# Performance work log

Measured on AMD Instinct MI355X. Metric: run time of the kernel, lower is better.

The kernel has to match this reference:

```python
import jax, jax.numpy as jnp
import numpy as np

VOCAB = 100000
EMBED = 64
B, S, K = 1024, 50, 20


def setup_inputs() -> dict:
    key = jax.random.key(0)
    k1, k2, k3 = jax.random.split(key, 3)
    content_input = jax.random.randint(k1, (B, S, K), 0, VOCAB)
    # nn.Linear(vocab_size, embed_size): weight [E, V], bias [E]
    W = jax.random.normal(k2, (EMBED, VOCAB), dtype=jnp.float32) * 0.02
    b = jax.random.normal(k3, (EMBED,), dtype=jnp.float32) * 0.02
    return {"content_input": content_input, "W": W, "b": b}


def reference(content_input, W, b):
    # Original: multi_hot = one_hot(ids, V).sum(2); out = multi_hot @ W.T + b
    # Mathematically identical gather-reduce: sum rows of W.T at ids, plus bias.
    # Duplicate ids are correctly counted because the one-hot sum accumulates counts.
    rows = jnp.take(W.T, content_input, axis=0)  # [B, S, K, E]
    return rows.sum(axis=2) + b                  # [B, S, E]
```

## Files before the change

### kernel.cpp

```cpp
#include <hip/hip_runtime.h>
#include <hip/hip_bf16.h>

#define VOCAB 100000
#define EMBED 64
#define NPAIR (1024 * 50)
#define KIDS  20

typedef int   int4v   __attribute__((ext_vector_type(4)));
typedef float float2v __attribute__((ext_vector_type(2)));

static __device__ inline ushort f2bf(float f) {
    __hip_bfloat16 h = __float2bfloat16(f);
    return __builtin_bit_cast(ushort, h);
}
static __device__ inline float bf2f(ushort u) {
    unsigned int v = ((unsigned int)u) << 16;
    return __builtin_bit_cast(float, v);
}

__global__ __launch_bounds__(256) void convert_w(const float* __restrict__ W,
                                                 ushort* __restrict__ Wt) {
    __shared__ float tile[64][65];
    const int v0 = blockIdx.x * 64;
    const int tx = threadIdx.x & 63;
    const int ty = threadIdx.x >> 6;
    const int v = v0 + tx;
    if (v < VOCAB) {
        #pragma unroll
        for (int e = ty; e < 64; e += 4) {
            tile[tx][e] = __builtin_nontemporal_load(&W[(size_t)e * VOCAB + v]);
        }
    }
    __syncthreads();
    const int r  = threadIdx.x >> 2;
    const int c0 = (threadIdx.x & 3) * 16;
    if (v0 + r < VOCAB) {
        uint pk[8];
        #pragma unroll
        for (int i = 0; i < 8; i++) {
            ushort lo = f2bf(tile[r][c0 + 2 * i + 0]);
            ushort hi = f2bf(tile[r][c0 + 2 * i + 1]);
            pk[i] = (uint)lo | ((uint)hi << 16);
        }
        uint4* outv = (uint4*)(Wt + (size_t)(v0 + r) * 64 + c0);
        outv[0] = make_uint4(pk[0], pk[1], pk[2], pk[3]);
        outv[1] = make_uint4(pk[4], pk[5], pk[6], pk[7]);
    }
}

__global__ __launch_bounds__(256) void gather_bf16(const int* __restrict__ ids,
                                                   const uint* __restrict__ Wt32,
                                                   const float* __restrict__ bias,
                                                   float* __restrict__ out) {
    const int wave = (blockIdx.x * blockDim.x + threadIdx.x) >> 6;
    const int lane = threadIdx.x & 63;
    if (wave >= NPAIR) return;

    const int h  = lane >> 5;
    const int ll = lane & 31;

    const int4v* idv = (const int4v*)(ids + (size_t)wave * KIDS);
    int4v q0 = __builtin_nontemporal_load(&idv[0]);
    int4v q1 = __builtin_nontemporal_load(&idv[1]);
    int4v q2 = __builtin_nontemporal_load(&idv[2]);
    int4v q3 = __builtin_nontemporal_load(&idv[3]);
    int4v q4 = __builtin_nontemporal_load(&idv[4]);

    uint u0 = Wt32[(((uint)(h ? q0.y : q0.x)) << 5) + ll];
    uint u1 = Wt32[(((uint)(h ? q0.w : q0.z)) << 5) + ll];
    uint u2 = Wt32[(((uint)(h ? q1.y : q1.x)) << 5) + ll];
    uint u3 = Wt32[(((uint)(h ? q1.w : q1.z)) << 5) + ll];
    uint u4 = Wt32[(((uint)(h ? q2.y : q2.x)) << 5) + ll];
    uint u5 = Wt32[(((uint)(h ? q2.w : q2.z)) << 5) + ll];
    uint u6 = Wt32[(((uint)(h ? q3.y : q3.x)) << 5) + ll];
    uint u7 = Wt32[(((uint)(h ? q3.w : q3.z)) << 5) + ll];
    uint u8 = Wt32[(((uint)(h ? q4.y : q4.x)) << 5) + ll];
    uint u9 = Wt32[(((uint)(h ? q4.w : q4.z)) << 5) + ll];

    float accE = 0.f, accO = 0.f;
    accE += bf2f((ushort)(u0 & 0xffff)); accO += bf2f((ushort)(u0 >> 16));
    accE += bf2f((ushort)(u1 & 0xffff)); accO += bf2f((ushort)(u1 >> 16));
    accE += bf2f((ushort)(u2 & 0xffff)); accO += bf2f((ushort)(u2 >> 16));
    accE += bf2f((ushort)(u3 & 0xffff)); accO += bf2f((ushort)(u3 >> 16));
    accE += bf2f((ushort)(u4 & 0xffff)); accO += bf2f((ushort)(u4 >> 16));
    accE += bf2f((ushort)(u5 & 0xffff)); accO += bf2f((ushort)(u5 >> 16));
    accE += bf2f((ushort)(u6 & 0xffff)); accO += bf2f((ushort)(u6 >> 16));
    accE += bf2f((ushort)(u7 & 0xffff)); accO += bf2f((ushort)(u7 >> 16));
    accE += bf2f((ushort)(u8 & 0xffff)); accO += bf2f((ushort)(u8 >> 16));
    accE += bf2f((ushort)(u9 & 0xffff)); accO += bf2f((ushort)(u9 >> 16));

    accE += __shfl_xor(accE, 32);
    accO += __shfl_xor(accO, 32);

    if (h == 0) {
        float2v bb = ((const float2v*)bias)[ll];
        float2v r;
        r.x = accE + bb.x;
        r.y = accO + bb.y;
        __builtin_nontemporal_store(r, &((float2v*)out)[(size_t)wave * 32 + ll]);
    }
}

__global__ __launch_bounds__(256) void gather_direct(const int* __restrict__ ids,
                                                     const float* __restrict__ W,
                                                     const float* __restrict__ bias,
                                                     float* __restrict__ out) {
    const int wave = (blockIdx.x * blockDim.x + threadIdx.x) >> 6;
    const int lane = threadIdx.x & 63;
    if (wave >= NPAIR) return;

    const int* myids = ids + (size_t)wave * KIDS;
    float acc = bias[lane];
    #pragma unroll
    for (int k = 0; k < KIDS; k++) {
        int id = myids[k];
        acc += W[(size_t)lane * VOCAB + id];
    }
    out[(size_t)wave * 64 + lane] = acc;
}

extern "C" void kernel_launch(void* const* d_in, const int* in_sizes, int n_in,
                              void* d_out, int out_size, void* d_ws, size_t ws_size,
                              hipStream_t stream) {
    const int*   ids  = (const int*)d_in[0];
    const float* W    = (const float*)d_in[1];
    const float* bias = (const float*)d_in[2];
    float*       out  = (float*)d_out;

    const size_t wt_bytes = (size_t)VOCAB * EMBED * sizeof(ushort);

    if (ws_size >= wt_bytes) {
        ushort* Wt = (ushort*)d_ws;
        const int tr_blocks = (VOCAB + 63) / 64;
        convert_w<<<tr_blocks, 256, 0, stream>>>(W, Wt);
        const int g_blocks = (NPAIR * 64 + 255) / 256;
        gather_bf16<<<g_blocks, 256, 0, stream>>>(ids, (const uint*)Wt, bias, out);
    } else {
        const int g_blocks = (NPAIR * 64 + 255) / 256;
        gather_direct<<<g_blocks, 256, 0, stream>>>(ids, W, bias, out);
    }
}
```

Before: 105.8 us.

## Map two output rows per wave, each half-wave gathering all ids

Restructures the bf16 gather so each 32-lane half-wave handles a whole (b,s) pair and sums all 20 rows itself, rather than splitting the ids across the two halves and combining them with a cross-half shuffle. The grid is halved and the shuffle and the masked store are dropped, so every lane writes output. The trade-off is a longer serial chain of dependent loads per lane, which leaves less memory-level parallelism per wave. Id loads also become plain loads instead of nontemporal ones.

```diff
diff --git a/kernel.cpp b/kernel.cpp
--- a/kernel.cpp
+++ b/kernel.cpp
@@ -52,53 +52,35 @@
                                                    const uint* __restrict__ Wt32,
                                                    const float* __restrict__ bias,
                                                    float* __restrict__ out) {
-    const int wave = (blockIdx.x * blockDim.x + threadIdx.x) >> 6;
+    const int pp   = (blockIdx.x * blockDim.x + threadIdx.x) >> 6;
     const int lane = threadIdx.x & 63;
-    if (wave >= NPAIR) return;
+    if (pp >= NPAIR / 2) return;
 
-    const int h  = lane >> 5;
-    const int ll = lane & 31;
+    const int h    = lane >> 5;
+    const int ll   = lane & 31;
+    const int pair = pp * 2 + h;
 
-    const int4v* idv = (const int4v*)(ids + (size_t)wave * KIDS);
-    int4v q0 = __builtin_nontemporal_load(&idv[0]);
-    int4v q1 = __builtin_nontemporal_load(&idv[1]);
-    int4v q2 = __builtin_nontemporal_load(&idv[2]);
-    int4v q3 = __builtin_nontemporal_load(&idv[3]);
-    int4v q4 = __builtin_nontemporal_load(&idv[4]);
-
-    uint u0 = Wt32[(((uint)(h ? q0.y : q0.x)) << 5) + ll];
-    uint u1 = Wt32[(((uint)(h ? q0.w : q0.z)) << 5) + ll];
-    uint u2 = Wt32[(((uint)(h ? q1.y : q1.x)) << 5) + ll];
-    uint u3 = Wt32[(((uint)(h ? q1.w : q1.z)) << 5) + ll];
-    uint u4 = Wt32[(((uint)(h ? q2.y : q2.x)) << 5) + ll];
-    uint u5 = Wt32[(((uint)(h ? q2.w : q2.z)) << 5) + ll];
-    uint u6 = Wt32[(((uint)(h ? q3.y : q3.x)) << 5) + ll];
-    uint u7 = Wt32[(((uint)(h ? q3.w : q3.z)) << 5) + ll];
-    uint u8 = Wt32[(((uint)(h ? q4.y : q4.x)) << 5) + ll];
-    uint u9 = Wt32[(((uint)(h ? q4.w : q4.z)) << 5) + ll];
+    const int4v* idv = (const int4v*)(ids + (size_t)pair * KIDS);
 
     float accE = 0.f, accO = 0.f;
-    accE += bf2f((ushort)(u0 & 0xffff)); accO += bf2f((ushort)(u0 >> 16));
-    accE += bf2f((ushort)(u1 & 0xffff)); accO += bf2f((ushort)(u1 >> 16));
-    accE += bf2f((ushort)(u2 & 0xffff)); accO += bf2f((ushort)(u2 >> 16));
-    accE += bf2f((ushort)(u3 & 0xffff)); accO += bf2f((ushort)(u3 >> 16));
-    accE += bf2f((ushort)(u4 & 0xffff)); accO += bf2f((ushort)(u4 >> 16));
-    accE += bf2f((ushort)(u5 & 0xffff)); accO += bf2f((ushort)(u5 >> 16));
-    accE += bf2f((ushort)(u6 & 0xffff)); accO += bf2f((ushort)(u6 >> 16));
-    accE += bf2f((ushort)(u7 & 0xffff)); accO += bf2f((ushort)(u7 >> 16));
-    accE += bf2f((ushort)(u8 & 0xffff)); accO += bf2f((ushort)(u8 >> 16));
-    accE += bf2f((ushort)(u9 & 0xffff)); accO += bf2f((ushort)(u9 >> 16));
+    #pragma unroll
+    for (int k = 0; k < 5; k++) {
+        int4v q = idv[k];
+        uint u0 = Wt32[(((uint)q.x) << 5) + ll];
+        uint u1 = Wt32[(((uint)q.y) << 5) + ll];
+        uint u2 = Wt32[(((uint)q.z) << 5) + ll];
+        uint u3 = Wt32[(((uint)q.w) << 5) + ll];
+        accE += bf2f((ushort)(u0 & 0xffff)); accO += bf2f((ushort)(u0 >> 16));
+        accE += bf2f((ushort)(u1 & 0xffff)); accO += bf2f((ushort)(u1 >> 16));
+        accE += bf2f((ushort)(u2 & 0xffff)); accO += bf2f((ushort)(u2 >> 16));
+        accE += bf2f((ushort)(u3 & 0xffff)); accO += bf2f((ushort)(u3 >> 16));
+    }
 
-    accE += __shfl_xor(accE, 32);
-    accO += __shfl_xor(accO, 32);
-
-    if (h == 0) {
-        float2v bb = ((const float2v*)bias)[ll];
-        float2v r;
-        r.x = accE + bb.x;
-        r.y = accO + bb.y;
-        __builtin_nontemporal_store(r, &((float2v*)out)[(size_t)wave * 32 + ll]);
-    }
+    float2v bb = ((const float2v*)bias)[ll];
+    float2v r;
+    r.x = accE + bb.x;
+    r.y = accO + bb.y;
+    __builtin_nontemporal_store(r, &((float2v*)out)[(size_t)pair * 32 + ll]);
 }
 
 __global__ __launch_bounds__(256) void gather_direct(const int* __restrict__ ids,
@@ -133,7 +115,7 @@
         ushort* Wt = (ushort*)d_ws;
         const int tr_blocks = (VOCAB + 63) / 64;
         convert_w<<<tr_blocks, 256, 0, stream>>>(W, Wt);
-        const int g_blocks = (NPAIR * 64 + 255) / 256;
+        const int g_blocks = ((NPAIR / 2) * 64 + 255) / 256;
         gather_bf16<<<g_blocks, 256, 0, stream>>>(ids, (const uint*)Wt, bias, out);
     } else {
         const int g_blocks = (NPAIR * 64 + 255) / 256;
```

Measured after the change: 103.4 us. -2.2%, faster.
